# Optimization experiments

Hardware: AMD Instinct MI355X
Metric: run time of the kernel (lower is better)

## Reference

```python
import jax, jax.numpy as jnp
import numpy as np

B, N, C = 8, 4096, 1024
H = 16
D = C // H  # head_dim = 64
SCALE = D ** -0.5


def setup_inputs() -> dict:
    key = jax.random.key(0)
    ks = jax.random.split(key, 5)
    std = C ** -0.5
    return {
        "x": jax.random.normal(ks[0], (B, N, C), dtype=jnp.float32),
        "Wq": jax.random.normal(ks[1], (C, C), dtype=jnp.float32) * std,
        "Wk": jax.random.normal(ks[2], (C, C), dtype=jnp.float32) * std,
        "Wv": jax.random.normal(ks[3], (C, C), dtype=jnp.float32) * std,
        "Wo": jax.random.normal(ks[4], (C, C), dtype=jnp.float32) * std,
        "bo": jnp.zeros((C,), dtype=jnp.float32),
    }


def reference(x, Wq, Wk, Wv, Wo, bo):
    b, n, c = x.shape
    # projections -> (B, N, H, D)
    q = (x @ Wq).reshape(b, n, H, D)
    k = (x @ Wk).reshape(b, n, H, D)
    v = (x @ Wv).reshape(b, n, H, D)
    # feature maps: softmax over head_dim for q, over sequence for k
    q = jax.nn.softmax(q, axis=-1) * SCALE
    k = jax.nn.softmax(k, axis=1)
    # O(N) linear attention: kv summary then apply to q
    kv = jnp.einsum("bnhf,bnhd->bhfd", k, v)   # (B, H, D, D)
    y = jnp.einsum("bnhf,bhfd->bnhd", q, kv)   # (B, N, H, D)
    y = y.reshape(b, n, H * D)
    return y @ Wo + bo
```

## Files before the change

kernel.cpp:

```cpp
#include <hip/hip_runtime.h>


typedef unsigned short u16;
typedef __bf16 bf16x8v __attribute__((ext_vector_type(8)));
typedef float f32x4 __attribute__((ext_vector_type(4)));
typedef u16 u16x8 __attribute__((ext_vector_type(8)));
typedef u16 u16x4 __attribute__((ext_vector_type(4)));

#define AS1C(p) (const __attribute__((address_space(1))) void*)(p)
#define AS3(p)  (__attribute__((address_space(3))) void*)(p)

__device__ __forceinline__ float b2f(u16 u) {
    union { unsigned u; float f; } c; c.u = ((unsigned)u) << 16; return c.f;
}
__device__ __forceinline__ u16 f2b(float f) {
    union { float f; unsigned u; } c; c.f = f;
    unsigned x = c.u + 0x7fffu + ((c.u >> 16) & 1u);
    return (u16)(x >> 16);
}

__global__ void prep(const float* __restrict__ x, u16* __restrict__ xb,
                     const float* __restrict__ Wq, const float* __restrict__ Wk,
                     const float* __restrict__ Wv, const float* __restrict__ Wo,
                     u16* __restrict__ wt, u16* __restrict__ wot) {
    if (blockIdx.x < 1024) {
        __shared__ float tl[64][65];
        const int which = blockIdx.x >> 8;
        const float* src = which == 0 ? Wq : which == 1 ? Wk : which == 2 ? Wv : Wo;
        u16* dst = which < 3 ? wt + which * 1048576 : wot;
        const int bx = blockIdx.x & 255;
        const int tx = bx & 15, ty = bx >> 4;
        const int j = threadIdx.x & 63, i0 = threadIdx.x >> 6;
        #pragma unroll
        for (int it = 0; it < 16; ++it) {
            int i = it * 4 + i0;
            tl[i][j] = src[(ty * 64 + i) * 1024 + tx * 64 + j];
        }
        __syncthreads();
        #pragma unroll
        for (int it = 0; it < 16; ++it) {
            int i = it * 4 + i0;
            dst[(tx * 64 + i) * 1024 + ty * 64 + j] = f2b(tl[j][i]);
        }
    } else {
        const long n4 = 8388608L;
        long i = (long)(blockIdx.x - 1024) * blockDim.x + threadIdx.x;
        long stride = 2048L * blockDim.x;
        for (long jj = i; jj < n4; jj += stride) {
            float4 v = ((const float4*)x)[jj];
            u16x4 o = { f2b(v.x), f2b(v.y), f2b(v.z), f2b(v.w) };
            ((u16x4*)xb)[jj] = o;
        }
    }
}

template<int OUTMODE>
__global__ __launch_bounds__(512, 2) void gemm256(
    const u16* __restrict__ A, const u16* __restrict__ Bt,
    void* __restrict__ Cout, const float* __restrict__ bias,
    const int lda, const int ldc, const int ntn, const int nwg)
{
    __shared__ __align__(16) u16 lds[65536];
    const int t = threadIdx.x;
    const int w = t >> 6, lane = t & 63;
    const int l16 = lane & 15, g = lane >> 4;
    const int wr = w >> 2, wc = w & 3;

    const int cpx = nwg >> 3;
    const int bid = blockIdx.x;
    const int swzb = (bid & 7) * cpx + (bid >> 3);
    const int tm = swzb / ntn, tn = swzb - tm * ntn;
    const long row0 = (long)tm << 8, col0 = (long)tn << 8;

    const int r0 = t >> 2;
    const int eo = (((t & 3) ^ ((t >> 3) & 3)) << 3);
    const u16* pa0 = A + (row0 + r0) * (long)lda + eo;
    const u16* pa1 = A + (row0 + 128 + r0) * (long)lda + eo;
    const u16* pb0 = Bt + (col0 + r0) * 1024L + eo;
    const u16* pb1 = Bt + (col0 + 128 + r0) * 1024L + eo;
    const int wB = w << 9;

#define STAGE_A(Tt) { const int _b = ((Tt)&3)*16384; const int _k = ((Tt)&31)*32;        \
    __builtin_amdgcn_global_load_lds(AS1C(pa0 + _k), AS3(lds + _b + wB), 16, 0, 0);      \
    __builtin_amdgcn_global_load_lds(AS1C(pa1 + _k), AS3(lds + _b + 4096 + wB), 16, 0, 0); }
#define STAGE_B(Tt) { const int _b = ((Tt)&3)*16384; const int _k = ((Tt)&31)*32;        \
    __builtin_amdgcn_global_load_lds(AS1C(pb0 + _k), AS3(lds + _b + 8192 + wB), 16, 0, 0);  \
    __builtin_amdgcn_global_load_lds(AS1C(pb1 + _k), AS3(lds + _b + 12288 + wB), 16, 0, 0); }

    STAGE_A(0); STAGE_B(0);
    STAGE_A(1); STAGE_B(1);
    STAGE_A(2); STAGE_B(2);

    f32x4 acc[8][4] = {};
    const int sw = ((g ^ ((l16 >> 1) & 3)) << 3);
    const int arow = wr * 128 + l16;

    #pragma unroll 4
    for (int T = 0; T < 32; ++T) {
        const int bufE = (T & 3) * 16384;
        const int Tn = T + 3;
        STAGE_A(Tn);
        asm volatile("s_waitcnt vmcnt(10)" ::: "memory");
        __builtin_amdgcn_s_barrier();
        __builtin_amdgcn_sched_barrier(0);
        bf16x8v bfr[4], afr[4];
        #pragma unroll
        for (int ni = 0; ni < 4; ++ni)
            bfr[ni] = __builtin_bit_cast(bf16x8v,
                *(const u16x8*)&lds[bufE + 8192 + ((wc * 64 + ni * 16 + l16) * 32) + sw]);
        #pragma unroll
        for (int mi = 0; mi < 4; ++mi)
            afr[mi] = __builtin_bit_cast(bf16x8v,
                *(const u16x8*)&lds[bufE + (arow + mi * 16) * 32 + sw]);
        __builtin_amdgcn_s_setprio(1);
        #pragma unroll
        for (int mi = 0; mi < 4; ++mi) {
            #pragma unroll
            for (int ni = 0; ni < 4; ++ni)
                acc[mi][ni] = __builtin_amdgcn_mfma_f32_16x16x32_bf16(
                    afr[mi], bfr[ni], acc[mi][ni], 0, 0, 0);
        }
        __builtin_amdgcn_s_setprio(0);
        STAGE_B(Tn);
        bf16x8v afr2[4];
        #pragma unroll
        for (int mi = 0; mi < 4; ++mi)
            afr2[mi] = __builtin_bit_cast(bf16x8v,
                *(const u16x8*)&lds[bufE + (arow + 64 + mi * 16) * 32 + sw]);
        __builtin_amdgcn_s_setprio(1);
        #pragma unroll
        for (int mi = 0; mi < 4; ++mi) {
            #pragma unroll
            for (int ni = 0; ni < 4; ++ni)
                acc[4 + mi][ni] = __builtin_amdgcn_mfma_f32_16x16x32_bf16(
                    afr2[mi], bfr[ni], acc[4 + mi][ni], 0, 0, 0);
        }
        __builtin_amdgcn_s_setprio(0);
        __builtin_amdgcn_s_barrier();
        __builtin_amdgcn_sched_barrier(0);
    }
    asm volatile("s_waitcnt vmcnt(0)" ::: "memory");
#undef STAGE_A
#undef STAGE_B

    const long crow = row0 + wr * 128 + g * 4;
    const long ccol = col0 + wc * 64 + l16;
    if (OUTMODE == 0) {
        u16* Cb = (u16*)Cout;
        #pragma unroll
        for (int mi = 0; mi < 8; ++mi) {
            #pragma unroll
            for (int ni = 0; ni < 4; ++ni) {
                long base = (crow + mi * 16) * (long)ldc + ccol + ni * 16;
                #pragma unroll
                for (int r = 0; r < 4; ++r)
                    Cb[base + (long)r * ldc] = f2b(acc[mi][ni][r]);
            }
        }
    } else {
        float* Cf = (float*)Cout;
        float bv[4];
        #pragma unroll
        for (int ni = 0; ni < 4; ++ni) bv[ni] = bias[ccol + ni * 16];
        #pragma unroll
        for (int mi = 0; mi < 8; ++mi) {
            #pragma unroll
            for (int ni = 0; ni < 4; ++ni) {
                long base = (crow + mi * 16) * (long)ldc + ccol + ni * 16;
                #pragma unroll
                for (int r = 0; r < 4; ++r)
                    Cf[base + (long)r * ldc] = acc[mi][ni][r] + bv[ni];
            }
        }
    }
}

__global__ __launch_bounds__(256) void kv_partial(const u16* __restrict__ qkv,
                                                  float* __restrict__ kvp,
                                                  float* __restrict__ psum) {
    __shared__ __align__(16) float kf_s[64 * 68];
    __shared__ __align__(16) float v_s[64 * 68];
    const int t = threadIdx.x;
    const int bx = blockIdx.x;
    const int nc = bx & 7, h = (bx >> 3) & 15, b = bx >> 7;
    const int f0 = (t >> 4) << 2;
    const int d0 = (t & 15) << 2;
    const int lr = t >> 3, lc = (t & 7) << 3;
    const long rowbase = (long)b * 4096 + nc * 512;
    const u16* kfg = qkv + (rowbase + lr) * 3072 + 1024 + h * 64 + lc;
    const u16* vg = kfg + 1024;
    float acc[4][4] = {};
    float cs[4] = {};
    for (int n0 = 0; n0 < 512; n0 += 64) {
        long go = (long)n0 * 3072;
        u16x8 kr0 = *(const u16x8*)(kfg + go);
        u16x8 kr1 = *(const u16x8*)(kfg + go + 32L * 3072);
        u16x8 vr0 = *(const u16x8*)(vg + go);
        u16x8 vr1 = *(const u16x8*)(vg + go + 32L * 3072);
        f32x4 ke0a, ke0b, ke1a, ke1b, vv0a, vv0b, vv1a, vv1b;
        #pragma unroll
        for (int j = 0; j < 4; ++j) {
            ke0a[j] = __expf(b2f(kr0[j]));     ke0b[j] = __expf(b2f(kr0[j + 4]));
            ke1a[j] = __expf(b2f(kr1[j]));     ke1b[j] = __expf(b2f(kr1[j + 4]));
            vv0a[j] = b2f(vr0[j]);             vv0b[j] = b2f(vr0[j + 4]);
            vv1a[j] = b2f(vr1[j]);             vv1b[j] = b2f(vr1[j + 4]);
        }
        *(f32x4*)&kf_s[lr * 68 + lc]            = ke0a;
        *(f32x4*)&kf_s[lr * 68 + lc + 4]        = ke0b;
        *(f32x4*)&kf_s[(lr + 32) * 68 + lc]     = ke1a;
        *(f32x4*)&kf_s[(lr + 32) * 68 + lc + 4] = ke1b;
        *(f32x4*)&v_s[lr * 68 + lc]             = vv0a;
        *(f32x4*)&v_s[lr * 68 + lc + 4]         = vv0b;
        *(f32x4*)&v_s[(lr + 32) * 68 + lc]      = vv1a;
        *(f32x4*)&v_s[(lr + 32) * 68 + lc + 4]  = vv1b;
        __syncthreads();
        #pragma unroll 8
        for (int r = 0; r < 64; ++r) {
            f32x4 kf4 = *(const f32x4*)&kf_s[r * 68 + f0];
            f32x4 vf4 = *(const f32x4*)&v_s[r * 68 + d0];
            #pragma unroll
            for (int i = 0; i < 4; ++i) {
                cs[i] += kf4[i];
                #pragma unroll
                for (int jj = 0; jj < 4; ++jj)
                    acc[i][jj] += kf4[i] * vf4[jj];
            }
        }
        __syncthreads();
    }
    float* o = kvp + (long)nc * 524288 + ((long)(b * 16 + h)) * 4096;
    #pragma unroll
    for (int i = 0; i < 4; ++i) {
        #pragma unroll
        for (int jj = 0; jj < 4; ++jj)
            o[(f0 + i) * 64 + d0 + jj] = acc[i][jj];
    }
    if ((t & 15) == 0) {
        float* ps = psum + ((long)nc * 128 + b * 16 + h) * 64 + f0;
        #pragma unroll
        for (int i = 0; i < 4; ++i) ps[i] = cs[i];
    }
}

__global__ void kv_combine_T(const float* __restrict__ kvp, const float* __restrict__ psum,
                             u16* __restrict__ kvTb) {
    __shared__ float tl[64 * 65];
    __shared__ float inv_s[64];
    const int bh = blockIdx.x;
    const int t = threadIdx.x;
    if (t < 64) {
        float s = 0.f;
        #pragma unroll
        for (int nc = 0; nc < 8; ++nc) s += psum[((long)nc * 128 + bh) * 64 + t];
        inv_s[t] = 1.0f / s;
    }
    __syncthreads();
    const float* p = kvp + (long)bh * 4096;
    #pragma unroll
    for (int it = 0; it < 16; ++it) {
        int idx = it * 256 + t;
        float v = 0.f;
        #pragma unroll
        for (int nc = 0; nc < 8; ++nc) v += p[(long)nc * 524288 + idx];
        tl[(idx & 63) * 65 + (idx >> 6)] = v * inv_s[idx >> 6];
    }
    __syncthreads();
    u16* o = kvTb + (long)bh * 4096;
    #pragma unroll
    for (int it = 0; it < 16; ++it) {
        int idx = it * 256 + t;
        o[idx] = f2b(tl[(idx >> 6) * 65 + (idx & 63)]);
    }
}

__global__ __launch_bounds__(256) void apply_mfma(u16* __restrict__ qkv,
                                                  const u16* __restrict__ kvTb) {
    __shared__ __align__(16) u16 Qs[8192];
    const int t = threadIdx.x;
    const int bx = blockIdx.x;
    const int nt = bx & 31, h = (bx >> 5) & 15, b = bx >> 9;
    const long n0 = (long)b * 4096 + (long)nt * 128;
    const int wave = t >> 6, lane = t & 63;
    const int wr = wave >> 1, wc = wave & 1;
    const int l16 = lane & 15, g = lane >> 4;

    const int colg = t & 7;
    const int rloc = t >> 3;
    #pragma unroll
    for (int p = 0; p < 4; ++p) {
        const int row = p * 32 + rloc;
        u16x8 qv = *(const u16x8*)(qkv + (n0 + row) * 3072 + h * 64 + colg * 8);
        float f[8];
        #pragma unroll
        for (int j = 0; j < 8; ++j) f[j] = b2f(qv[j]);
        float m = f[0];
        #pragma unroll
        for (int j = 1; j < 8; ++j) m = fmaxf(m, f[j]);
        m = fmaxf(m, __shfl_xor(m, 1)); m = fmaxf(m, __shfl_xor(m, 2)); m = fmaxf(m, __shfl_xor(m, 4));
        float s = 0.f;
        #pragma unroll
        for (int j = 0; j < 8; ++j) { f[j] = __expf(f[j] - m); s += f[j]; }
        s += __shfl_xor(s, 1); s += __shfl_xor(s, 2); s += __shfl_xor(s, 4);
        const float sc = 0.125f / s;
        u16x8 ov;
        #pragma unroll
        for (int j = 0; j < 8; ++j) ov[j] = f2b(f[j] * sc);
        const int chunk = colg ^ (row & 7);
        *(u16x8*)&Qs[row * 64 + chunk * 8] = ov;
    }
    __syncthreads();

    const u16* kvb = kvTb + ((long)(b * 16 + h) << 12);
    bf16x8v bkv[2][2];
    #pragma unroll
    for (int ni = 0; ni < 2; ++ni) {
        #pragma unroll
        for (int ks = 0; ks < 2; ++ks)
            bkv[ni][ks] = __builtin_bit_cast(bf16x8v,
                *(const u16x8*)(kvb + (wc * 32 + ni * 16 + l16) * 64 + ks * 32 + g * 8));
    }
    bf16x8v aq[4][2];
    #pragma unroll
    for (int mi = 0; mi < 4; ++mi) {
        const int row = wr * 64 + mi * 16 + l16;
        #pragma unroll
        for (int ks = 0; ks < 2; ++ks) {
            const int c16 = (ks * 4 + g) ^ (row & 7);
            aq[mi][ks] = __builtin_bit_cast(bf16x8v,
                *(const u16x8*)&Qs[row * 64 + c16 * 8]);
        }
    }
    f32x4 acc[4][2] = {};
    #pragma unroll
    for (int mi = 0; mi < 4; ++mi) {
        #pragma unroll
        for (int ni = 0; ni < 2; ++ni) {
            acc[mi][ni] = __builtin_amdgcn_mfma_f32_16x16x32_bf16(
                aq[mi][0], bkv[ni][0], acc[mi][ni], 0, 0, 0);
            acc[mi][ni] = __builtin_amdgcn_mfma_f32_16x16x32_bf16(
                aq[mi][1], bkv[ni][1], acc[mi][ni], 0, 0, 0);
        }
    }
    #pragma unroll
    for (int mi = 0; mi < 4; ++mi) {
        #pragma unroll
        for (int ni = 0; ni < 2; ++ni) {
            long row = n0 + wr * 64 + mi * 16 + g * 4;
            int col = h * 64 + wc * 32 + ni * 16 + l16;
            #pragma unroll
            for (int r = 0; r < 4; ++r)
                qkv[(row + r) * 3072 + col] = f2b(acc[mi][ni][r]);
        }
    }
}

extern "C" void kernel_launch(void* const* d_in, const int* in_sizes, int n_in,
                              void* d_out, int out_size, void* d_ws, size_t ws_size,
                              hipStream_t stream) {
    (void)in_sizes; (void)n_in; (void)out_size; (void)ws_size;
    const float* x  = (const float*)d_in[0];
    const float* Wq = (const float*)d_in[1];
    const float* Wk = (const float*)d_in[2];
    const float* Wv = (const float*)d_in[3];
    const float* Wo = (const float*)d_in[4];
    const float* bo = (const float*)d_in[5];

    u16* xb  = (u16*)d_ws;
    u16* wt  = xb + 33554432;
    u16* wot = wt + 3145728;
    u16* qkv = wot + 1048576;
    u16*   kvTb = qkv + 100663296;
    float* kvp  = (float*)xb;
    float* psum = kvp + 4194304;

    prep<<<3072, 256, 0, stream>>>(x, xb, Wq, Wk, Wv, Wo, wt, wot);
    gemm256<0><<<1536, 512, 0, stream>>>(xb, wt, (void*)qkv, nullptr, 1024, 3072, 12, 1536);
    kv_partial<<<1024, 256, 0, stream>>>(qkv, kvp, psum);
    kv_combine_T<<<128, 256, 0, stream>>>(kvp, psum, kvTb);
    apply_mfma<<<4096, 256, 0, stream>>>(qkv, kvTb);
    gemm256<1><<<512, 512, 0, stream>>>(qkv, wot, d_out, bo, 3072, 1024, 4, 512);
}
```

Before: 435.8 us.

## Restructure GEMM mainloop with BK=64 double buffer and fuse Q softmax

The bf16 GEMM mainloop changes from four 32-wide K buffers to two 64-wide K buffers with an 8-chunk XOR swizzle. Global-to-LDS loads are now interleaved across four MFMA sub-phases, each separated by a barrier, to overlap memory with compute and halve the number of K iterations. Separately, the per-head softmax over q is moved into the QKV GEMM epilogue (OUTMODE 2, for column tiles below 1024), so apply_mfma now copies q directly into LDS. The new schedule adds more barriers per iteration and relies on carefully tuned vmcnt counts for correctness.

```diff
diff --git a/kernel.cpp b/kernel.cpp
--- a/kernel.cpp
+++ b/kernel.cpp
@@ -72,80 +72,107 @@
     const int tm = swzb / ntn, tn = swzb - tm * ntn;
     const long row0 = (long)tm << 8, col0 = (long)tn << 8;
 
-    const int r0 = t >> 2;
-    const int eo = (((t & 3) ^ ((t >> 3) & 3)) << 3);
-    const u16* pa0 = A + (row0 + r0) * (long)lda + eo;
-    const u16* pa1 = A + (row0 + 128 + r0) * (long)lda + eo;
-    const u16* pb0 = Bt + (col0 + r0) * 1024L + eo;
-    const u16* pb1 = Bt + (col0 + 128 + r0) * 1024L + eo;
-    const int wB = w << 9;
-
-#define STAGE_A(Tt) { const int _b = ((Tt)&3)*16384; const int _k = ((Tt)&31)*32;        \
-    __builtin_amdgcn_global_load_lds(AS1C(pa0 + _k), AS3(lds + _b + wB), 16, 0, 0);      \
-    __builtin_amdgcn_global_load_lds(AS1C(pa1 + _k), AS3(lds + _b + 4096 + wB), 16, 0, 0); }
-#define STAGE_B(Tt) { const int _b = ((Tt)&3)*16384; const int _k = ((Tt)&31)*32;        \
-    __builtin_amdgcn_global_load_lds(AS1C(pb0 + _k), AS3(lds + _b + 8192 + wB), 16, 0, 0);  \
-    __builtin_amdgcn_global_load_lds(AS1C(pb1 + _k), AS3(lds + _b + 12288 + wB), 16, 0, 0); }
-
-    STAGE_A(0); STAGE_B(0);
-    STAGE_A(1); STAGE_B(1);
-    STAGE_A(2); STAGE_B(2);
-
+    const int eo = (((t & 7) ^ ((t >> 3) & 7)) << 3);
+    const u16* pA = A + (row0 + (t >> 3)) * (long)lda + eo;
+    const u16* pB = Bt + (col0 + (t >> 3)) * 1024L + eo;
+    const long a64 = (long)lda << 6;
+
+#define STG_A(Tt, j) __builtin_amdgcn_global_load_lds(                        \
+    AS1C(pA + (long)(j) * a64 + (((Tt) & 15) << 6)),                          \
+    AS3(lds + ((((Tt) & 1) << 15) + ((j) << 12) + t * 8)), 16, 0, 0);
+#define STG_B(Tt, j) __builtin_amdgcn_global_load_lds(                        \
+    AS1C(pB + (long)(j) * 65536L + (((Tt) & 15) << 6)),                       \
+    AS3(lds + ((((Tt) & 1) << 15) + 16384 + ((j) << 12) + t * 8)), 16, 0, 0);
+
+    const int swz = l16 & 7;
+    const int koff0 = ((0 * 4 + g) ^ swz) << 3;
+    const int koff1 = ((1 * 4 + g) ^ swz) << 3;
+    const int arow = ((wr << 7) + l16) << 6;
+    const int brow = 16384 + (((wc << 6) + l16) << 6);
+
+    u16x8 aM[4][2], b0[2][2], b1[2][2];
     f32x4 acc[8][4] = {};
-    const int sw = ((g ^ ((l16 >> 1) & 3)) << 3);
-    const int arow = wr * 128 + l16;
-
-    #pragma unroll 4
-    for (int T = 0; T < 32; ++T) {
-        const int bufE = (T & 3) * 16384;
-        const int Tn = T + 3;
-        STAGE_A(Tn);
-        asm volatile("s_waitcnt vmcnt(10)" ::: "memory");
+
+#define RD_A(half) { _Pragma("unroll") for (int mi = 0; mi < 4; ++mi) {       \
+    const int ab = bufE + arow + ((half) * 64 + mi * 16) * 64;                \
+    aM[mi][0] = *(const u16x8*)&lds[ab + koff0];                              \
+    aM[mi][1] = *(const u16x8*)&lds[ab + koff1]; } }
+#define RD_B(nh, br) { _Pragma("unroll") for (int ni = 0; ni < 2; ++ni) {     \
+    const int bb = bufE + brow + ((nh) * 32 + ni * 16) * 64;                  \
+    br[ni][0] = *(const u16x8*)&lds[bb + koff0];                              \
+    br[ni][1] = *(const u16x8*)&lds[bb + koff1]; } }
+#define MM(mh, nh, br) { __builtin_amdgcn_s_setprio(1);                       \
+    _Pragma("unroll") for (int mi = 0; mi < 4; ++mi)                          \
+    { _Pragma("unroll") for (int ni = 0; ni < 2; ++ni) {                      \
+    f32x4 c = acc[(mh)*4 + mi][(nh)*2 + ni];                                  \
+    c = __builtin_amdgcn_mfma_f32_16x16x32_bf16(                              \
+        __builtin_bit_cast(bf16x8v, aM[mi][0]),                               \
+        __builtin_bit_cast(bf16x8v, br[ni][0]), c, 0, 0, 0);                  \
+    c = __builtin_amdgcn_mfma_f32_16x16x32_bf16(                              \
+        __builtin_bit_cast(bf16x8v, aM[mi][1]),                               \
+        __builtin_bit_cast(bf16x8v, br[ni][1]), c, 0, 0, 0);                  \
+    acc[(mh)*4 + mi][(nh)*2 + ni] = c; } }                                    \
+    __builtin_amdgcn_s_setprio(0); }
+
+    STG_A(0, 0) STG_A(0, 2) STG_B(0, 0) STG_B(0, 1)
+    STG_B(0, 2) STG_B(0, 3) STG_A(0, 1) STG_A(0, 3)
+    STG_A(1, 0) STG_A(1, 2) STG_B(1, 0) STG_B(1, 1)
+    asm volatile("s_waitcnt vmcnt(6)" ::: "memory");
+    __builtin_amdgcn_s_barrier();
+
+    #pragma unroll 2
+    for (int T = 0; T < 16; ++T) {
+        const int bufE = (T & 1) << 15;
+        RD_A(0) RD_B(0, b0)
+        STG_B(T + 1, 2) STG_B(T + 1, 3)
         __builtin_amdgcn_s_barrier();
-        __builtin_amdgcn_sched_barrier(0);
-        bf16x8v bfr[4], afr[4];
-        #pragma unroll
-        for (int ni = 0; ni < 4; ++ni)
-            bfr[ni] = __builtin_bit_cast(bf16x8v,
-                *(const u16x8*)&lds[bufE + 8192 + ((wc * 64 + ni * 16 + l16) * 32) + sw]);
-        #pragma unroll
-        for (int mi = 0; mi < 4; ++mi)
-            afr[mi] = __builtin_bit_cast(bf16x8v,
-                *(const u16x8*)&lds[bufE + (arow + mi * 16) * 32 + sw]);
-        __builtin_amdgcn_s_setprio(1);
-        #pragma unroll
-        for (int mi = 0; mi < 4; ++mi) {
-            #pragma unroll
-            for (int ni = 0; ni < 4; ++ni)
-                acc[mi][ni] = __builtin_amdgcn_mfma_f32_16x16x32_bf16(
-                    afr[mi], bfr[ni], acc[mi][ni], 0, 0, 0);
-        }
-        __builtin_amdgcn_s_setprio(0);
-        STAGE_B(Tn);
-        bf16x8v afr2[4];
-        #pragma unroll
-        for (int mi = 0; mi < 4; ++mi)
-            afr2[mi] = __builtin_bit_cast(bf16x8v,
-                *(const u16x8*)&lds[bufE + (arow + 64 + mi * 16) * 32 + sw]);
-        __builtin_amdgcn_s_setprio(1);
-        #pragma unroll
-        for (int mi = 0; mi < 4; ++mi) {
-            #pragma unroll
-            for (int ni = 0; ni < 4; ++ni)
-                acc[4 + mi][ni] = __builtin_amdgcn_mfma_f32_16x16x32_bf16(
-                    afr2[mi], bfr[ni], acc[4 + mi][ni], 0, 0, 0);
-        }
-        __builtin_amdgcn_s_setprio(0);
+        MM(0, 0, b0)
+        RD_B(1, b1)
+        STG_A(T + 1, 1) STG_A(T + 1, 3)
+        asm volatile("s_waitcnt vmcnt(8)" ::: "memory");
         __builtin_amdgcn_s_barrier();
-        __builtin_amdgcn_sched_barrier(0);
+        MM(0, 1, b1)
+        RD_A(1)
+        STG_A(T + 2, 0) STG_A(T + 2, 2)
+        __builtin_amdgcn_s_barrier();
+        MM(1, 0, b0)
+        STG_B(T + 2, 0) STG_B(T + 2, 1)
+        asm volatile("s_waitcnt vmcnt(6)" ::: "memory");
+        __builtin_amdgcn_s_barrier();
+        MM(1, 1, b1)
     }
     asm volatile("s_waitcnt vmcnt(0)" ::: "memory");
-#undef STAGE_A
-#undef STAGE_B
+#undef STG_A
+#undef STG_B
+#undef RD_A
+#undef RD_B
+#undef MM
+
+    if (OUTMODE == 2 && tn < 4) {
+        #pragma unroll
+        for (int mi = 0; mi < 8; ++mi) {
+            #pragma unroll
+            for (int r = 0; r < 4; ++r) {
+                float v0 = acc[mi][0][r], v1 = acc[mi][1][r];
+                float v2 = acc[mi][2][r], v3 = acc[mi][3][r];
+                float m = fmaxf(fmaxf(v0, v1), fmaxf(v2, v3));
+                m = fmaxf(m, __shfl_xor(m, 1)); m = fmaxf(m, __shfl_xor(m, 2));
+                m = fmaxf(m, __shfl_xor(m, 4)); m = fmaxf(m, __shfl_xor(m, 8));
+                v0 = __expf(v0 - m); v1 = __expf(v1 - m);
+                v2 = __expf(v2 - m); v3 = __expf(v3 - m);
+                float s = v0 + v1 + v2 + v3;
+                s += __shfl_xor(s, 1); s += __shfl_xor(s, 2);
+                s += __shfl_xor(s, 4); s += __shfl_xor(s, 8);
+                const float sc = 0.125f / s;
+                acc[mi][0][r] = v0 * sc; acc[mi][1][r] = v1 * sc;
+                acc[mi][2][r] = v2 * sc; acc[mi][3][r] = v3 * sc;
+            }
+        }
+    }
 
     const long crow = row0 + wr * 128 + g * 4;
     const long ccol = col0 + wc * 64 + l16;
-    if (OUTMODE == 0) {
+    if (OUTMODE != 1) {
         u16* Cb = (u16*)Cout;
         #pragma unroll
         for (int mi = 0; mi < 8; ++mi) {
@@ -290,23 +317,8 @@
     for (int p = 0; p < 4; ++p) {
         const int row = p * 32 + rloc;
         u16x8 qv = *(const u16x8*)(qkv + (n0 + row) * 3072 + h * 64 + colg * 8);
-        float f[8];
-        #pragma unroll
-        for (int j = 0; j < 8; ++j) f[j] = b2f(qv[j]);
-        float m = f[0];
-        #pragma unroll
-        for (int j = 1; j < 8; ++j) m = fmaxf(m, f[j]);
-        m = fmaxf(m, __shfl_xor(m, 1)); m = fmaxf(m, __shfl_xor(m, 2)); m = fmaxf(m, __shfl_xor(m, 4));
-        float s = 0.f;
-        #pragma unroll
-        for (int j = 0; j < 8; ++j) { f[j] = __expf(f[j] - m); s += f[j]; }
-        s += __shfl_xor(s, 1); s += __shfl_xor(s, 2); s += __shfl_xor(s, 4);
-        const float sc = 0.125f / s;
-        u16x8 ov;
-        #pragma unroll
-        for (int j = 0; j < 8; ++j) ov[j] = f2b(f[j] * sc);
         const int chunk = colg ^ (row & 7);
-        *(u16x8*)&Qs[row * 64 + chunk * 8] = ov;
+        *(u16x8*)&Qs[row * 64 + chunk * 8] = qv;
     }
     __syncthreads();
 
@@ -374,7 +386,7 @@
     float* psum = kvp + 4194304;
 
     prep<<<3072, 256, 0, stream>>>(x, xb, Wq, Wk, Wv, Wo, wt, wot);
-    gemm256<0><<<1536, 512, 0, stream>>>(xb, wt, (void*)qkv, nullptr, 1024, 3072, 12, 1536);
+    gemm256<2><<<1536, 512, 0, stream>>>(xb, wt, (void*)qkv, nullptr, 1024, 3072, 12, 1536);
     kv_partial<<<1024, 256, 0, stream>>>(qkv, kvp, psum);
     kv_combine_T<<<128, 256, 0, stream>>>(kvp, psum, kvTb);
     apply_mfma<<<4096, 256, 0, stream>>>(qkv, kvTb);
```

Measured after the change: 417.2 us. -4.3%, faster.

## Fuse q softmax and k exp into QKV GEMM epilogue; restructure load pipeline

Applied to the files above, without the earlier changes.

Adds a GEMM output mode that applies the per-head softmax (scaled) to the Q columns and exp to the K columns before storing bf16. kv_partial and apply_mfma then skip those element-wise passes. The main loop also issues all four tile loads together after the MFMAs, with a single wait and barrier, instead of splitting them around the two MFMA halves. Storing exp(k) in bf16 without max subtraction risks overflow and precision loss. The epilogue adds shuffles and exps to the GEMM tail.

```diff
diff --git a/kernel.cpp b/kernel.cpp
--- a/kernel.cpp
+++ b/kernel.cpp
@@ -80,49 +80,33 @@
     const u16* pb1 = Bt + (col0 + 128 + r0) * 1024L + eo;
     const int wB = w << 9;
 
-#define STAGE_A(Tt) { const int _b = ((Tt)&3)*16384; const int _k = ((Tt)&31)*32;        \
-    __builtin_amdgcn_global_load_lds(AS1C(pa0 + _k), AS3(lds + _b + wB), 16, 0, 0);      \
-    __builtin_amdgcn_global_load_lds(AS1C(pa1 + _k), AS3(lds + _b + 4096 + wB), 16, 0, 0); }
-#define STAGE_B(Tt) { const int _b = ((Tt)&3)*16384; const int _k = ((Tt)&31)*32;        \
+#define STAGE(Tt) { const int _b = ((Tt)&3)*16384; const int _k = ((Tt)&31)*32;             \
+    __builtin_amdgcn_global_load_lds(AS1C(pa0 + _k), AS3(lds + _b + wB), 16, 0, 0);         \
+    __builtin_amdgcn_global_load_lds(AS1C(pa1 + _k), AS3(lds + _b + 4096 + wB), 16, 0, 0);  \
     __builtin_amdgcn_global_load_lds(AS1C(pb0 + _k), AS3(lds + _b + 8192 + wB), 16, 0, 0);  \
     __builtin_amdgcn_global_load_lds(AS1C(pb1 + _k), AS3(lds + _b + 12288 + wB), 16, 0, 0); }
 
-    STAGE_A(0); STAGE_B(0);
-    STAGE_A(1); STAGE_B(1);
-    STAGE_A(2); STAGE_B(2);
+    STAGE(0) STAGE(1) STAGE(2)
+    asm volatile("s_waitcnt vmcnt(8)" ::: "memory");
+    __builtin_amdgcn_s_barrier();
 
     f32x4 acc[8][4] = {};
     const int sw = ((g ^ ((l16 >> 1) & 3)) << 3);
     const int arow = wr * 128 + l16;
+    const int brow = wc * 64 + l16;
 
     #pragma unroll 4
     for (int T = 0; T < 32; ++T) {
         const int bufE = (T & 3) * 16384;
-        const int Tn = T + 3;
-        STAGE_A(Tn);
-        asm volatile("s_waitcnt vmcnt(10)" ::: "memory");
-        __builtin_amdgcn_s_barrier();
-        __builtin_amdgcn_sched_barrier(0);
-        bf16x8v bfr[4], afr[4];
+        bf16x8v bfr[4], afr[4], afr2[4];
         #pragma unroll
         for (int ni = 0; ni < 4; ++ni)
             bfr[ni] = __builtin_bit_cast(bf16x8v,
-                *(const u16x8*)&lds[bufE + 8192 + ((wc * 64 + ni * 16 + l16) * 32) + sw]);
+                *(const u16x8*)&lds[bufE + 8192 + (brow + ni * 16) * 32 + sw]);
         #pragma unroll
         for (int mi = 0; mi < 4; ++mi)
             afr[mi] = __builtin_bit_cast(bf16x8v,
                 *(const u16x8*)&lds[bufE + (arow + mi * 16) * 32 + sw]);
-        __builtin_amdgcn_s_setprio(1);
-        #pragma unroll
-        for (int mi = 0; mi < 4; ++mi) {
-            #pragma unroll
-            for (int ni = 0; ni < 4; ++ni)
-                acc[mi][ni] = __builtin_amdgcn_mfma_f32_16x16x32_bf16(
-                    afr[mi], bfr[ni], acc[mi][ni], 0, 0, 0);
-        }
-        __builtin_amdgcn_s_setprio(0);
-        STAGE_B(Tn);
-        bf16x8v afr2[4];
         #pragma unroll
         for (int mi = 0; mi < 4; ++mi)
             afr2[mi] = __builtin_bit_cast(bf16x8v,
@@ -132,20 +116,58 @@
         for (int mi = 0; mi < 4; ++mi) {
             #pragma unroll
             for (int ni = 0; ni < 4; ++ni)
+                acc[mi][ni] = __builtin_amdgcn_mfma_f32_16x16x32_bf16(
+                    afr[mi], bfr[ni], acc[mi][ni], 0, 0, 0);
+        }
+        #pragma unroll
+        for (int mi = 0; mi < 4; ++mi) {
+            #pragma unroll
+            for (int ni = 0; ni < 4; ++ni)
                 acc[4 + mi][ni] = __builtin_amdgcn_mfma_f32_16x16x32_bf16(
                     afr2[mi], bfr[ni], acc[4 + mi][ni], 0, 0, 0);
         }
         __builtin_amdgcn_s_setprio(0);
+        STAGE(T + 3)
+        asm volatile("s_waitcnt vmcnt(8)" ::: "memory");
         __builtin_amdgcn_s_barrier();
-        __builtin_amdgcn_sched_barrier(0);
     }
     asm volatile("s_waitcnt vmcnt(0)" ::: "memory");
-#undef STAGE_A
-#undef STAGE_B
+#undef STAGE
+
+    if (OUTMODE == 2 && tn < 4) {
+        #pragma unroll
+        for (int mi = 0; mi < 8; ++mi) {
+            #pragma unroll
+            for (int r = 0; r < 4; ++r) {
+                float v0 = acc[mi][0][r], v1 = acc[mi][1][r];
+                float v2 = acc[mi][2][r], v3 = acc[mi][3][r];
+                float m = fmaxf(fmaxf(v0, v1), fmaxf(v2, v3));
+                m = fmaxf(m, __shfl_xor(m, 1)); m = fmaxf(m, __shfl_xor(m, 2));
+                m = fmaxf(m, __shfl_xor(m, 4)); m = fmaxf(m, __shfl_xor(m, 8));
+                v0 = __expf(v0 - m); v1 = __expf(v1 - m);
+                v2 = __expf(v2 - m); v3 = __expf(v3 - m);
+                float s = v0 + v1 + v2 + v3;
+                s += __shfl_xor(s, 1); s += __shfl_xor(s, 2);
+                s += __shfl_xor(s, 4); s += __shfl_xor(s, 8);
+                const float sc = 0.125f / s;
+                acc[mi][0][r] = v0 * sc; acc[mi][1][r] = v1 * sc;
+                acc[mi][2][r] = v2 * sc; acc[mi][3][r] = v3 * sc;
+            }
+        }
+    }
+    if (OUTMODE == 2 && tn >= 4 && tn < 8) {
+        #pragma unroll
+        for (int mi = 0; mi < 8; ++mi)
+            #pragma unroll
+            for (int ni = 0; ni < 4; ++ni)
+                #pragma unroll
+                for (int r = 0; r < 4; ++r)
+                    acc[mi][ni][r] = __expf(acc[mi][ni][r]);
+    }
 
     const long crow = row0 + wr * 128 + g * 4;
     const long ccol = col0 + wc * 64 + l16;
-    if (OUTMODE == 0) {
+    if (OUTMODE != 1) {
         u16* Cb = (u16*)Cout;
         #pragma unroll
         for (int mi = 0; mi < 8; ++mi) {
@@ -200,10 +222,10 @@
         f32x4 ke0a, ke0b, ke1a, ke1b, vv0a, vv0b, vv1a, vv1b;
         #pragma unroll
         for (int j = 0; j < 4; ++j) {
-            ke0a[j] = __expf(b2f(kr0[j]));     ke0b[j] = __expf(b2f(kr0[j + 4]));
-            ke1a[j] = __expf(b2f(kr1[j]));     ke1b[j] = __expf(b2f(kr1[j + 4]));
-            vv0a[j] = b2f(vr0[j]);             vv0b[j] = b2f(vr0[j + 4]);
-            vv1a[j] = b2f(vr1[j]);             vv1b[j] = b2f(vr1[j + 4]);
+            ke0a[j] = b2f(kr0[j]);     ke0b[j] = b2f(kr0[j + 4]);
+            ke1a[j] = b2f(kr1[j]);     ke1b[j] = b2f(kr1[j + 4]);
+            vv0a[j] = b2f(vr0[j]);     vv0b[j] = b2f(vr0[j + 4]);
+            vv1a[j] = b2f(vr1[j]);     vv1b[j] = b2f(vr1[j + 4]);
         }
         *(f32x4*)&kf_s[lr * 68 + lc]            = ke0a;
         *(f32x4*)&kf_s[lr * 68 + lc + 4]        = ke0b;
@@ -290,23 +312,8 @@
     for (int p = 0; p < 4; ++p) {
         const int row = p * 32 + rloc;
         u16x8 qv = *(const u16x8*)(qkv + (n0 + row) * 3072 + h * 64 + colg * 8);
-        float f[8];
-        #pragma unroll
-        for (int j = 0; j < 8; ++j) f[j] = b2f(qv[j]);
-        float m = f[0];
-        #pragma unroll
-        for (int j = 1; j < 8; ++j) m = fmaxf(m, f[j]);
-        m = fmaxf(m, __shfl_xor(m, 1)); m = fmaxf(m, __shfl_xor(m, 2)); m = fmaxf(m, __shfl_xor(m, 4));
-        float s = 0.f;
-        #pragma unroll
-        for (int j = 0; j < 8; ++j) { f[j] = __expf(f[j] - m); s += f[j]; }
-        s += __shfl_xor(s, 1); s += __shfl_xor(s, 2); s += __shfl_xor(s, 4);
-        const float sc = 0.125f / s;
-        u16x8 ov;
-        #pragma unroll
-        for (int j = 0; j < 8; ++j) ov[j] = f2b(f[j] * sc);
         const int chunk = colg ^ (row & 7);
-        *(u16x8*)&Qs[row * 64 + chunk * 8] = ov;
+        *(u16x8*)&Qs[row * 64 + chunk * 8] = qv;
     }
     __syncthreads();
 
@@ -374,7 +381,7 @@
     float* psum = kvp + 4194304;
 
     prep<<<3072, 256, 0, stream>>>(x, xb, Wq, Wk, Wv, Wo, wt, wot);
-    gemm256<0><<<1536, 512, 0, stream>>>(xb, wt, (void*)qkv, nullptr, 1024, 3072, 12, 1536);
+    gemm256<2><<<1536, 512, 0, stream>>>(xb, wt, (void*)qkv, nullptr, 1024, 3072, 12, 1536);
     kv_partial<<<1024, 256, 0, stream>>>(qkv, kvp, psum);
     kv_combine_T<<<128, 256, 0, stream>>>(kvp, psum, kvTb);
     apply_mfma<<<4096, 256, 0, stream>>>(qkv, kvTb);
```

Measured after the change: 449.5 us. 1.03x slower.
